# Kernel optimization log

Measured on AMD Instinct MI355X. Metric: run time of the kernel, lower is better.

## Reference

```python
import jax, jax.numpy as jnp
import numpy as np

HIDDEN = 1024
HEADS = 16
HEAD_DIM = HIDDEN // HEADS


def setup_inputs() -> dict:
    key = jax.random.key(0)
    ks = jax.random.split(key, 7)
    B, S = 4, 2048
    xav = float(np.sqrt(6.0 / (HIDDEN + HIDDEN)))  # xavier uniform bound
    def lin(k):
        return jax.random.uniform(k, (HIDDEN, HIDDEN), jnp.float32, -xav, xav)
    return {
        "hidden_states": jax.random.normal(ks[0], (B, S, HIDDEN), jnp.float32),
        "Wq": lin(ks[1]), "bq": jnp.zeros((HIDDEN,), jnp.float32),
        "Wk": lin(ks[2]), "bk": jnp.zeros((HIDDEN,), jnp.float32),
        "Wv": lin(ks[3]), "bv": jnp.zeros((HIDDEN,), jnp.float32),
    }


def reference(hidden_states, Wq, bq, Wk, bk, Wv, bv):
    B, S, H = hidden_states.shape
    def split_heads(t):  # [B,S,H] -> [B,heads,S,head_dim]
        return t.reshape(B, S, HEADS, HEAD_DIM).transpose(0, 2, 1, 3)
    q = split_heads(hidden_states @ Wq + bq)
    k = split_heads(hidden_states @ Wk + bk)
    v = split_heads(hidden_states @ Wv + bv)
    scores = jnp.einsum("bhqd,bhkd->bhqk", q, k) / jnp.sqrt(
        jnp.asarray(HEAD_DIM, hidden_states.dtype))
    probs = jax.nn.softmax(scores, axis=-1)  # dropout p=0.0 (inference)
    ctx = jnp.einsum("bhqk,bhkd->bhqd", probs, v)
    ctx = ctx.transpose(0, 2, 1, 3).reshape(B, S, H)
    return ctx
```

## Files before the change

kernel.cpp:

```cpp
#include <hip/hip_runtime.h>
#include <hip/hip_bf16.h>
#include <cstdint>

#define HIDDEN 1024
#define HEADS 16
#define HDIM 64
#define BATCH 4
#define SEQ 2048
#define MTOT (BATCH * SEQ)

typedef __attribute__((ext_vector_type(8))) short bfrag;
typedef __attribute__((ext_vector_type(4))) float cfrag;
typedef __attribute__((ext_vector_type(4))) float float4v;
typedef __attribute__((ext_vector_type(4))) unsigned short ushort4v;
typedef __attribute__((ext_vector_type(2))) unsigned int uint2v;

#define AS1 __attribute__((address_space(1)))
#define AS3 __attribute__((address_space(3)))

__device__ __forceinline__ void gl_lds16(const void* g, void* l) {
  __builtin_amdgcn_global_load_lds((AS1 void*)g, (AS3 void*)l, 16, 0, 0);
}

__device__ __forceinline__ uint16_t f2b(float f) {
  union { float f; uint32_t u; } v; v.f = f;
  uint32_t u = v.u;
  return (uint16_t)((u + 0x7FFFu + ((u >> 16) & 1u)) >> 16);
}

__global__ __launch_bounds__(256) void cvt_kernel(
    const float* __restrict__ x, const float* __restrict__ W0,
    const float* __restrict__ W1, const float* __restrict__ W2,
    uint16_t* __restrict__ Xb, uint16_t* __restrict__ Wt) {
  int bid = blockIdx.x;
  if (bid < 4096) {
    int i = bid * 256 + threadIdx.x;
    float4v a = ((const float4v*)x)[2 * i];
    float4v b = ((const float4v*)x)[2 * i + 1];
    bfrag o;
    o[0] = (short)f2b(a[0]); o[1] = (short)f2b(a[1]);
    o[2] = (short)f2b(a[2]); o[3] = (short)f2b(a[3]);
    o[4] = (short)f2b(b[0]); o[5] = (short)f2b(b[1]);
    o[6] = (short)f2b(b[2]); o[7] = (short)f2b(b[3]);
    ((bfrag*)Xb)[i] = o;
    return;
  }
  int id = bid - 4096;
  int z = id >> 8, rem = id & 255;
  const float* W = z == 0 ? W0 : (z == 1 ? W1 : W2);
  uint16_t* out = Wt + (size_t)z * HIDDEN * HIDDEN;
  __shared__ float tile[64][65];
  int n0 = (rem & 15) * 64, k0 = (rem >> 4) * 64;
  int t = threadIdx.x;
  int r = t >> 2, cq = (t & 3) * 16;
#pragma unroll
  for (int i = 0; i < 16; i += 4) {
    float4v v = *(const float4v*)&W[(size_t)(k0 + r) * HIDDEN + n0 + cq + i];
    tile[r][cq + i + 0] = v[0]; tile[r][cq + i + 1] = v[1];
    tile[r][cq + i + 2] = v[2]; tile[r][cq + i + 3] = v[3];
  }
  __syncthreads();
  bfrag o0, o1;
#pragma unroll
  for (int i = 0; i < 8; ++i) o0[i] = (short)f2b(tile[cq + i][r]);
#pragma unroll
  for (int i = 0; i < 8; ++i) o1[i] = (short)f2b(tile[cq + 8 + i][r]);
  *(bfrag*)&out[(size_t)(n0 + r) * HIDDEN + k0 + cq] = o0;
  *(bfrag*)&out[(size_t)(n0 + r) * HIDDEN + k0 + cq + 8] = o1;
}

__global__ __launch_bounds__(256) void gemm_qkv_kernel(
    const uint16_t* __restrict__ X, const uint16_t* __restrict__ Wt,
    const float* __restrict__ b0, const float* __restrict__ b1,
    const float* __restrict__ b2,
    uint16_t* __restrict__ Qo, uint16_t* __restrict__ Ko, uint16_t* __restrict__ Vo) {
  __shared__ uint16_t As[2][128 * 32];
  __shared__ uint16_t Bs[2][128 * 32];

  int id = blockIdx.x;
  int xcd = id & 7, j = id >> 3;
  int which = j >> 6;
  int r_ = j & 63;
  int m0 = (xcd * 8 + (r_ >> 3)) * 128;
  int n0 = (r_ & 7) * 128;

  const uint16_t* Wp = Wt + (size_t)which * HIDDEN * HIDDEN;
  const float* bias = which == 0 ? b0 : (which == 1 ? b1 : b2);

  int tid = threadIdx.x;
  int wave = tid >> 6, lane = tid & 63;
  int wm = wave >> 1, wn = wave & 1;
  int g = lane >> 4, c = lane & 15;
  int sr = lane >> 2;
  int sc = (lane & 3) * 8;

  cfrag acc[4][4];
#pragma unroll
  for (int i = 0; i < 4; ++i)
#pragma unroll
    for (int jj = 0; jj < 4; ++jj) acc[i][jj] = cfrag{0.f, 0.f, 0.f, 0.f};

  auto STAGE = [&](int buf, int kt) {
    int kc = kt * 32 + sc;
#pragma unroll
    for (int i = 0; i < 2; ++i) {
      int rowA = (i * 4 + wave) * 16;
      gl_lds16(&X[(size_t)(m0 + rowA + sr) * HIDDEN + kc], &As[buf][rowA * 32]);
      gl_lds16(&Wp[(size_t)(n0 + rowA + sr) * HIDDEN + kc], &Bs[buf][rowA * 32]);
    }
  };

  STAGE(0, 0);
  __syncthreads();
  int cur = 0;

  for (int kt = 0; kt < HIDDEN / 32; ++kt) {
    if (kt < HIDDEN / 32 - 1) STAGE(cur ^ 1, kt + 1);
    bfrag af[4], bf[4];
#pragma unroll
    for (int mt = 0; mt < 4; ++mt)
      af[mt] = *(const bfrag*)&As[cur][(wm * 64 + mt * 16 + c) * 32 + g * 8];
#pragma unroll
    for (int nt = 0; nt < 4; ++nt)
      bf[nt] = *(const bfrag*)&Bs[cur][(wn * 64 + nt * 16 + c) * 32 + g * 8];
    __builtin_amdgcn_s_setprio(1);
#pragma unroll
    for (int mt = 0; mt < 4; ++mt)
#pragma unroll
      for (int nt = 0; nt < 4; ++nt)
        acc[mt][nt] = __builtin_amdgcn_mfma_f32_16x16x32_bf16(af[mt], bf[nt],
                                                              acc[mt][nt], 0, 0, 0);
    __builtin_amdgcn_s_setprio(0);
    __syncthreads();
    cur ^= 1;
  }

  if (which == 2) {
    int bb_ = m0 >> 11;
    int s0 = (m0 & 2047) + wm * 64;
#pragma unroll
    for (int nt = 0; nt < 4; ++nt) {
      int n = n0 + wn * 64 + nt * 16 + c;
      int h = n >> 6, d = n & 63;
      float bb = bias[n];
      size_t base = ((size_t)(bb_ * 16 + h) * 64 + d) * SEQ;
#pragma unroll
      for (int mt = 0; mt < 4; ++mt) {
        int s = s0 + mt * 16 + g * 4;
        ushort4v pk;
        pk[0] = f2b(acc[mt][nt][0] + bb);
        pk[1] = f2b(acc[mt][nt][1] + bb);
        pk[2] = f2b(acc[mt][nt][2] + bb);
        pk[3] = f2b(acc[mt][nt][3] + bb);
        *(ushort4v*)&Vo[base + s] = pk;
      }
    }
  } else {
    uint16_t* out = which == 0 ? Qo : Ko;
    float sc_ = which == 0 ? 0.125f * 1.44269504088896f : 1.0f;
#pragma unroll
    for (int nt = 0; nt < 4; ++nt) {
      int n = n0 + wn * 64 + nt * 16 + c;
      float bb = bias[n];
#pragma unroll
      for (int mt = 0; mt < 4; ++mt) {
        int mb = m0 + wm * 64 + mt * 16 + g * 4;
#pragma unroll
        for (int r = 0; r < 4; ++r)
          out[(size_t)(mb + r) * HIDDEN + n] = f2b((acc[mt][nt][r] + bb) * sc_);
      }
    }
  }
}

__global__ __launch_bounds__(256, 4) void attn_kernel(
    const uint16_t* __restrict__ Q, const uint16_t* __restrict__ K,
    const uint16_t* __restrict__ VT, float* __restrict__ out) {
  __shared__ uint16_t Ks[2][64 * 64];
  __shared__ uint16_t Vs[2][64 * 64];
  __shared__ __align__(16) uint16_t Pl[4][16][64];

  int bid = blockIdx.x;
  int wg = (bid & 7) * 256 + (bid >> 3);
  int bh = wg >> 5, qt = wg & 31;
  int b = bh >> 4, h = bh & 15;
  int tid = threadIdx.x, wave = tid >> 6, lane = tid & 63;
  int g = lane >> 4, c = lane & 15;
  size_t rowb = (size_t)b * SEQ;
  int colb = h * HDIM;
  const uint16_t* Kh = K + rowb * HIDDEN + colb;
  const uint16_t* Vh = VT + (size_t)bh * HDIM * SEQ;

  int r8 = lane >> 3, c8 = lane & 7;
  int scol = ((c8 ^ r8) << 3);
  int sbrow = (wave & 1) * 32;

  int qrow = qt * 64 + wave * 16 + c;
  bfrag aq[2];
  aq[0] = *(const bfrag*)&Q[(rowb + qrow) * HIDDEN + colb + g * 8];
  aq[1] = *(const bfrag*)&Q[(rowb + qrow) * HIDDEN + colb + 32 + g * 8];

  float mr = -INFINITY, lr = 0.f;
  cfrag oacc[4];
#pragma unroll
  for (int dt = 0; dt < 4; ++dt) oacc[dt] = cfrag{0.f, 0.f, 0.f, 0.f};

  if (wave < 2) {
#pragma unroll
    for (int j = 0; j < 4; ++j) {
      int rl = sbrow + j * 8;
      gl_lds16(&Kh[(size_t)(rl + r8) * HIDDEN + scol], &Ks[0][rl * 64]);
    }
  } else {
#pragma unroll
    for (int j = 0; j < 4; ++j) {
      int rl = sbrow + j * 8;
      gl_lds16(&Vh[(size_t)(rl + r8) * SEQ + scol], &Vs[0][rl * 64]);
    }
  }
  __syncthreads();

  int cur = 0;
  int sw = (c & 7) << 4;
  uint8_t* Pb = (uint8_t*)Pl + wave * 2048 + c * 128;

  for (int t = 0; t < 32; ++t) {
    int j0 = t * 64;
    if (t < 31) {
      int jn = j0 + 64;
      if (wave < 2) {
#pragma unroll
        for (int j = 0; j < 4; ++j) {
          int rl = sbrow + j * 8;
          gl_lds16(&Kh[(size_t)(jn + rl + r8) * HIDDEN + scol],
                   &Ks[cur ^ 1][rl * 64]);
        }
      } else {
#pragma unroll
        for (int j = 0; j < 4; ++j) {
          int rl = sbrow + j * 8;
          gl_lds16(&Vh[(size_t)(rl + r8) * SEQ + jn + scol],
                   &Vs[cur ^ 1][rl * 64]);
        }
      }
    }

    const uint8_t* Kbuf = (const uint8_t*)Ks[cur];
    const uint8_t* Vbuf = (const uint8_t*)Vs[cur];

    cfrag s[4];
#pragma unroll
    for (int nt = 0; nt < 4; ++nt) s[nt] = cfrag{0.f, 0.f, 0.f, 0.f};
    __builtin_amdgcn_s_setprio(1);
#pragma unroll
    for (int kb = 0; kb < 2; ++kb) {
#pragma unroll
      for (int nt = 0; nt < 4; ++nt) {
        int off = ((nt * 16 + c) * 128 + kb * 64 + g * 16) ^ sw;
        bfrag bk = *(const bfrag*)(Kbuf + off);
        s[nt] = __builtin_amdgcn_mfma_f32_16x16x32_bf16(bk, aq[kb], s[nt], 0, 0, 0);
      }
    }
    __builtin_amdgcn_s_setprio(0);

    float mx = fmaxf(fmaxf(s[0][0], s[0][1]), s[0][2]);
    mx = fmaxf(fmaxf(mx, s[0][3]), s[1][0]);
    mx = fmaxf(fmaxf(mx, s[1][1]), s[1][2]);
    mx = fmaxf(fmaxf(mx, s[1][3]), s[2][0]);
    mx = fmaxf(fmaxf(mx, s[2][1]), s[2][2]);
    mx = fmaxf(fmaxf(mx, s[2][3]), s[3][0]);
    mx = fmaxf(fmaxf(mx, s[3][1]), s[3][2]);
    mx = fmaxf(mx, s[3][3]);
    mx = fmaxf(mx, __shfl_xor(mx, 16, 64));
    mx = fmaxf(mx, __shfl_xor(mx, 32, 64));
    if (mx > mr + 8.0f) {
      float alpha = __builtin_amdgcn_exp2f(mr - mx);
      lr *= alpha;
#pragma unroll
      for (int dt = 0; dt < 4; ++dt)
#pragma unroll
        for (int r = 0; r < 4; ++r) oacc[dt][r] *= alpha;
      mr = mx;
    }
    float ps = 0.f;
#pragma unroll
    for (int nt = 0; nt < 4; ++nt) {
#pragma unroll
      for (int r = 0; r < 4; ++r)
        s[nt][r] = __builtin_amdgcn_exp2f(s[nt][r] - mr);
      ps += (s[nt][0] + s[nt][1]) + (s[nt][2] + s[nt][3]);
    }
    lr += ps;

#pragma unroll
    for (int nt = 0; nt < 4; ++nt) {
      uint32_t w0, w1;
      asm("v_cvt_pk_bf16_f32 %0, %1, %2" : "=v"(w0) : "v"(s[nt][0]), "v"(s[nt][1]));
      asm("v_cvt_pk_bf16_f32 %0, %1, %2" : "=v"(w1) : "v"(s[nt][2]), "v"(s[nt][3]));
      uint2v pw; pw[0] = w0; pw[1] = w1;
      *(uint2v*)(Pb + ((nt * 32 + g * 8) ^ sw)) = pw;
    }

    __builtin_amdgcn_s_setprio(1);
#pragma unroll
    for (int kb = 0; kb < 2; ++kb) {
      bfrag ap = *(const bfrag*)(Pb + ((kb * 64 + g * 16) ^ sw));
#pragma unroll
      for (int dt = 0; dt < 4; ++dt) {
        int off = ((dt * 16 + c) * 128 + kb * 64 + g * 16) ^ sw;
        bfrag bv = *(const bfrag*)(Vbuf + off);
        oacc[dt] = __builtin_amdgcn_mfma_f32_16x16x32_bf16(bv, ap, oacc[dt], 0, 0, 0);
      }
    }
    __builtin_amdgcn_s_setprio(0);

    __syncthreads();
    cur ^= 1;
  }

  lr += __shfl_xor(lr, 16, 64);
  lr += __shfl_xor(lr, 32, 64);
  float inv = 1.0f / lr;
  size_t orow = rowb + (size_t)qt * 64 + wave * 16 + c;
#pragma unroll
  for (int dt = 0; dt < 4; ++dt) {
    float4v o;
    o[0] = oacc[dt][0] * inv; o[1] = oacc[dt][1] * inv;
    o[2] = oacc[dt][2] * inv; o[3] = oacc[dt][3] * inv;
    *(float4v*)&out[orow * HIDDEN + colb + dt * 16 + g * 4] = o;
  }
}

extern "C" void kernel_launch(void* const* d_in, const int* in_sizes, int n_in,
                              void* d_out, int out_size, void* d_ws, size_t ws_size,
                              hipStream_t stream) {
  const float* x  = (const float*)d_in[0];
  const float* Wq = (const float*)d_in[1];
  const float* bq = (const float*)d_in[2];
  const float* Wk = (const float*)d_in[3];
  const float* bk = (const float*)d_in[4];
  const float* Wv = (const float*)d_in[5];
  const float* bv = (const float*)d_in[6];
  float* out = (float*)d_out;

  uint8_t* ws = (uint8_t*)d_ws;
  const size_t XB = 0;
  const size_t WT = XB + (size_t)MTOT * HIDDEN * 2;
  const size_t QB = WT + (size_t)3 * HIDDEN * HIDDEN * 2;
  const size_t KB = QB + (size_t)MTOT * HIDDEN * 2;
  const size_t VB = KB + (size_t)MTOT * HIDDEN * 2;
  uint16_t* Xb = (uint16_t*)(ws + XB);
  uint16_t* Wt = (uint16_t*)(ws + WT);
  uint16_t* Qb = (uint16_t*)(ws + QB);
  uint16_t* Kb = (uint16_t*)(ws + KB);
  uint16_t* Vb = (uint16_t*)(ws + VB);

  cvt_kernel<<<dim3(4096 + 768), 256, 0, stream>>>(x, Wq, Wk, Wv, Xb, Wt);
  gemm_qkv_kernel<<<dim3(1536), 256, 0, stream>>>(Xb, Wt, bq, bk, bv, Qb, Kb, Vb);
  attn_kernel<<<dim3(2048), 256, 0, stream>>>(Qb, Kb, Vb, out);
}
```

Measured before the change: 284.7 us.

## Double query rows per attention wave and simplify QKV GEMM to single-buffered grid

The attention kernel now has each wave handle 32 query rows as two 16-row halves. Each K/V tile loaded into LDS is reused across twice as many queries, which halves the grid and the K/V traffic per query. The cost is more registers, so occupancy drops from 4 to 3 blocks. The QKV GEMM goes the other way: it drops double-buffered LDS prefetch, the XCD-aware block remap and the priority hints in favour of a plain 3D grid, which exposes global-to-LDS load latency on every k-step.

```diff
diff --git a/kernel.cpp b/kernel.cpp
--- a/kernel.cpp
+++ b/kernel.cpp
@@ -74,19 +74,13 @@
     const float* __restrict__ b0, const float* __restrict__ b1,
     const float* __restrict__ b2,
     uint16_t* __restrict__ Qo, uint16_t* __restrict__ Ko, uint16_t* __restrict__ Vo) {
-  __shared__ uint16_t As[2][128 * 32];
-  __shared__ uint16_t Bs[2][128 * 32];
-
-  int id = blockIdx.x;
-  int xcd = id & 7, j = id >> 3;
-  int which = j >> 6;
-  int r_ = j & 63;
-  int m0 = (xcd * 8 + (r_ >> 3)) * 128;
-  int n0 = (r_ & 7) * 128;
-
+  __shared__ uint16_t As[128 * 32];
+  __shared__ uint16_t Bs[128 * 32];
+  int which = blockIdx.z;
   const uint16_t* Wp = Wt + (size_t)which * HIDDEN * HIDDEN;
   const float* bias = which == 0 ? b0 : (which == 1 ? b1 : b2);
 
+  int m0 = blockIdx.x * 128, n0 = blockIdx.y * 128;
   int tid = threadIdx.x;
   int wave = tid >> 6, lane = tid & 63;
   int wm = wave >> 1, wn = wave & 1;
@@ -100,39 +94,29 @@
 #pragma unroll
     for (int jj = 0; jj < 4; ++jj) acc[i][jj] = cfrag{0.f, 0.f, 0.f, 0.f};
 
-  auto STAGE = [&](int buf, int kt) {
+  for (int kt = 0; kt < HIDDEN / 32; ++kt) {
     int kc = kt * 32 + sc;
 #pragma unroll
     for (int i = 0; i < 2; ++i) {
       int rowA = (i * 4 + wave) * 16;
-      gl_lds16(&X[(size_t)(m0 + rowA + sr) * HIDDEN + kc], &As[buf][rowA * 32]);
-      gl_lds16(&Wp[(size_t)(n0 + rowA + sr) * HIDDEN + kc], &Bs[buf][rowA * 32]);
-    }
-  };
-
-  STAGE(0, 0);
-  __syncthreads();
-  int cur = 0;
-
-  for (int kt = 0; kt < HIDDEN / 32; ++kt) {
-    if (kt < HIDDEN / 32 - 1) STAGE(cur ^ 1, kt + 1);
+      gl_lds16(&X[(size_t)(m0 + rowA + sr) * HIDDEN + kc], &As[rowA * 32]);
+      gl_lds16(&Wp[(size_t)(n0 + rowA + sr) * HIDDEN + kc], &Bs[rowA * 32]);
+    }
+    __syncthreads();
     bfrag af[4], bf[4];
 #pragma unroll
     for (int mt = 0; mt < 4; ++mt)
-      af[mt] = *(const bfrag*)&As[cur][(wm * 64 + mt * 16 + c) * 32 + g * 8];
+      af[mt] = *(const bfrag*)&As[(wm * 64 + mt * 16 + c) * 32 + g * 8];
 #pragma unroll
     for (int nt = 0; nt < 4; ++nt)
-      bf[nt] = *(const bfrag*)&Bs[cur][(wn * 64 + nt * 16 + c) * 32 + g * 8];
-    __builtin_amdgcn_s_setprio(1);
+      bf[nt] = *(const bfrag*)&Bs[(wn * 64 + nt * 16 + c) * 32 + g * 8];
 #pragma unroll
     for (int mt = 0; mt < 4; ++mt)
 #pragma unroll
       for (int nt = 0; nt < 4; ++nt)
         acc[mt][nt] = __builtin_amdgcn_mfma_f32_16x16x32_bf16(af[mt], bf[nt],
                                                               acc[mt][nt], 0, 0, 0);
-    __builtin_amdgcn_s_setprio(0);
     __syncthreads();
-    cur ^= 1;
   }
 
   if (which == 2) {
@@ -173,16 +157,16 @@
   }
 }
 
-__global__ __launch_bounds__(256, 4) void attn_kernel(
+__global__ __launch_bounds__(256, 3) void attn_kernel(
     const uint16_t* __restrict__ Q, const uint16_t* __restrict__ K,
     const uint16_t* __restrict__ VT, float* __restrict__ out) {
   __shared__ uint16_t Ks[2][64 * 64];
   __shared__ uint16_t Vs[2][64 * 64];
-  __shared__ __align__(16) uint16_t Pl[4][16][64];
+  __shared__ __align__(16) uint16_t Pl[4][32][64];
 
   int bid = blockIdx.x;
-  int wg = (bid & 7) * 256 + (bid >> 3);
-  int bh = wg >> 5, qt = wg & 31;
+  int wg = (bid & 7) * 128 + (bid >> 3);
+  int bh = wg >> 4, qt = wg & 15;
   int b = bh >> 4, h = bh & 15;
   int tid = threadIdx.x, wave = tid >> 6, lane = tid & 63;
   int g = lane >> 4, c = lane & 15;
@@ -195,15 +179,22 @@
   int scol = ((c8 ^ r8) << 3);
   int sbrow = (wave & 1) * 32;
 
-  int qrow = qt * 64 + wave * 16 + c;
-  bfrag aq[2];
-  aq[0] = *(const bfrag*)&Q[(rowb + qrow) * HIDDEN + colb + g * 8];
-  aq[1] = *(const bfrag*)&Q[(rowb + qrow) * HIDDEN + colb + 32 + g * 8];
-
-  float mr = -INFINITY, lr = 0.f;
-  cfrag oacc[4];
-#pragma unroll
-  for (int dt = 0; dt < 4; ++dt) oacc[dt] = cfrag{0.f, 0.f, 0.f, 0.f};
+  int qrow = qt * 128 + wave * 32 + c;
+  bfrag aq0[2], aq1[2];
+#pragma unroll
+  for (int kb = 0; kb < 2; ++kb) {
+    aq0[kb] = *(const bfrag*)&Q[(rowb + qrow) * HIDDEN + colb + kb * 32 + g * 8];
+    aq1[kb] = *(const bfrag*)&Q[(rowb + qrow + 16) * HIDDEN + colb + kb * 32 + g * 8];
+  }
+
+  float mr0 = -INFINITY, lr0 = 0.f;
+  float mr1 = -INFINITY, lr1 = 0.f;
+  cfrag oacc0[4], oacc1[4];
+#pragma unroll
+  for (int dt = 0; dt < 4; ++dt) {
+    oacc0[dt] = cfrag{0.f, 0.f, 0.f, 0.f};
+    oacc1[dt] = cfrag{0.f, 0.f, 0.f, 0.f};
+  }
 
   if (wave < 2) {
 #pragma unroll
@@ -222,7 +213,8 @@
 
   int cur = 0;
   int sw = (c & 7) << 4;
-  uint8_t* Pb = (uint8_t*)Pl + wave * 2048 + c * 128;
+  uint8_t* Pb0 = (uint8_t*)Pl + wave * 4096 + c * 128;
+  uint8_t* Pb1 = Pb0 + 16 * 128;
 
   for (int t = 0; t < 32; ++t) {
     int j0 = t * 64;
@@ -248,9 +240,12 @@
     const uint8_t* Kbuf = (const uint8_t*)Ks[cur];
     const uint8_t* Vbuf = (const uint8_t*)Vs[cur];
 
-    cfrag s[4];
-#pragma unroll
-    for (int nt = 0; nt < 4; ++nt) s[nt] = cfrag{0.f, 0.f, 0.f, 0.f};
+    cfrag s0[4], s1[4];
+#pragma unroll
+    for (int nt = 0; nt < 4; ++nt) {
+      s0[nt] = cfrag{0.f, 0.f, 0.f, 0.f};
+      s1[nt] = cfrag{0.f, 0.f, 0.f, 0.f};
+    }
     __builtin_amdgcn_s_setprio(1);
 #pragma unroll
     for (int kb = 0; kb < 2; ++kb) {
@@ -258,58 +253,100 @@
       for (int nt = 0; nt < 4; ++nt) {
         int off = ((nt * 16 + c) * 128 + kb * 64 + g * 16) ^ sw;
         bfrag bk = *(const bfrag*)(Kbuf + off);
-        s[nt] = __builtin_amdgcn_mfma_f32_16x16x32_bf16(bk, aq[kb], s[nt], 0, 0, 0);
+        s0[nt] = __builtin_amdgcn_mfma_f32_16x16x32_bf16(bk, aq0[kb], s0[nt], 0, 0, 0);
+        s1[nt] = __builtin_amdgcn_mfma_f32_16x16x32_bf16(bk, aq1[kb], s1[nt], 0, 0, 0);
       }
     }
     __builtin_amdgcn_s_setprio(0);
 
-    float mx = fmaxf(fmaxf(s[0][0], s[0][1]), s[0][2]);
-    mx = fmaxf(fmaxf(mx, s[0][3]), s[1][0]);
-    mx = fmaxf(fmaxf(mx, s[1][1]), s[1][2]);
-    mx = fmaxf(fmaxf(mx, s[1][3]), s[2][0]);
-    mx = fmaxf(fmaxf(mx, s[2][1]), s[2][2]);
-    mx = fmaxf(fmaxf(mx, s[2][3]), s[3][0]);
-    mx = fmaxf(fmaxf(mx, s[3][1]), s[3][2]);
-    mx = fmaxf(mx, s[3][3]);
-    mx = fmaxf(mx, __shfl_xor(mx, 16, 64));
-    mx = fmaxf(mx, __shfl_xor(mx, 32, 64));
-    if (mx > mr + 8.0f) {
-      float alpha = __builtin_amdgcn_exp2f(mr - mx);
-      lr *= alpha;
-#pragma unroll
-      for (int dt = 0; dt < 4; ++dt)
-#pragma unroll
-        for (int r = 0; r < 4; ++r) oacc[dt][r] *= alpha;
-      mr = mx;
-    }
-    float ps = 0.f;
-#pragma unroll
-    for (int nt = 0; nt < 4; ++nt) {
-#pragma unroll
-      for (int r = 0; r < 4; ++r)
-        s[nt][r] = __builtin_amdgcn_exp2f(s[nt][r] - mr);
-      ps += (s[nt][0] + s[nt][1]) + (s[nt][2] + s[nt][3]);
-    }
-    lr += ps;
-
-#pragma unroll
-    for (int nt = 0; nt < 4; ++nt) {
-      uint32_t w0, w1;
-      asm("v_cvt_pk_bf16_f32 %0, %1, %2" : "=v"(w0) : "v"(s[nt][0]), "v"(s[nt][1]));
-      asm("v_cvt_pk_bf16_f32 %0, %1, %2" : "=v"(w1) : "v"(s[nt][2]), "v"(s[nt][3]));
-      uint2v pw; pw[0] = w0; pw[1] = w1;
-      *(uint2v*)(Pb + ((nt * 32 + g * 8) ^ sw)) = pw;
+    {
+      float mx = fmaxf(fmaxf(s0[0][0], s0[0][1]), s0[0][2]);
+      mx = fmaxf(fmaxf(mx, s0[0][3]), s0[1][0]);
+      mx = fmaxf(fmaxf(mx, s0[1][1]), s0[1][2]);
+      mx = fmaxf(fmaxf(mx, s0[1][3]), s0[2][0]);
+      mx = fmaxf(fmaxf(mx, s0[2][1]), s0[2][2]);
+      mx = fmaxf(fmaxf(mx, s0[2][3]), s0[3][0]);
+      mx = fmaxf(fmaxf(mx, s0[3][1]), s0[3][2]);
+      mx = fmaxf(mx, s0[3][3]);
+      mx = fmaxf(mx, __shfl_xor(mx, 16, 64));
+      mx = fmaxf(mx, __shfl_xor(mx, 32, 64));
+      if (mx > mr0 + 8.0f) {
+        float alpha = __builtin_amdgcn_exp2f(mr0 - mx);
+        lr0 *= alpha;
+#pragma unroll
+        for (int dt = 0; dt < 4; ++dt)
+#pragma unroll
+          for (int r = 0; r < 4; ++r) oacc0[dt][r] *= alpha;
+        mr0 = mx;
+      }
+      float ps = 0.f;
+#pragma unroll
+      for (int nt = 0; nt < 4; ++nt) {
+#pragma unroll
+        for (int r = 0; r < 4; ++r)
+          s0[nt][r] = __builtin_amdgcn_exp2f(s0[nt][r] - mr0);
+        ps += (s0[nt][0] + s0[nt][1]) + (s0[nt][2] + s0[nt][3]);
+      }
+      lr0 += ps;
+#pragma unroll
+      for (int nt = 0; nt < 4; ++nt) {
+        uint32_t w0, w1;
+        asm("v_cvt_pk_bf16_f32 %0, %1, %2" : "=v"(w0) : "v"(s0[nt][0]), "v"(s0[nt][1]));
+        asm("v_cvt_pk_bf16_f32 %0, %1, %2" : "=v"(w1) : "v"(s0[nt][2]), "v"(s0[nt][3]));
+        uint2v pw; pw[0] = w0; pw[1] = w1;
+        *(uint2v*)(Pb0 + ((nt * 32 + g * 8) ^ sw)) = pw;
+      }
+    }
+    {
+      float mx = fmaxf(fmaxf(s1[0][0], s1[0][1]), s1[0][2]);
+      mx = fmaxf(fmaxf(mx, s1[0][3]), s1[1][0]);
+      mx = fmaxf(fmaxf(mx, s1[1][1]), s1[1][2]);
+      mx = fmaxf(fmaxf(mx, s1[1][3]), s1[2][0]);
+      mx = fmaxf(fmaxf(mx, s1[2][1]), s1[2][2]);
+      mx = fmaxf(fmaxf(mx, s1[2][3]), s1[3][0]);
+      mx = fmaxf(fmaxf(mx, s1[3][1]), s1[3][2]);
+      mx = fmaxf(mx, s1[3][3]);
+      mx = fmaxf(mx, __shfl_xor(mx, 16, 64));
+      mx = fmaxf(mx, __shfl_xor(mx, 32, 64));
+      if (mx > mr1 + 8.0f) {
+        float alpha = __builtin_amdgcn_exp2f(mr1 - mx);
+        lr1 *= alpha;
+#pragma unroll
+        for (int dt = 0; dt < 4; ++dt)
+#pragma unroll
+          for (int r = 0; r < 4; ++r) oacc1[dt][r] *= alpha;
+        mr1 = mx;
+      }
+      float ps = 0.f;
+#pragma unroll
+      for (int nt = 0; nt < 4; ++nt) {
+#pragma unroll
+        for (int r = 0; r < 4; ++r)
+          s1[nt][r] = __builtin_amdgcn_exp2f(s1[nt][r] - mr1);
+        ps += (s1[nt][0] + s1[nt][1]) + (s1[nt][2] + s1[nt][3]);
+      }
+      lr1 += ps;
+#pragma unroll
+      for (int nt = 0; nt < 4; ++nt) {
+        uint32_t w0, w1;
+        asm("v_cvt_pk_bf16_f32 %0, %1, %2" : "=v"(w0) : "v"(s1[nt][0]), "v"(s1[nt][1]));
+        asm("v_cvt_pk_bf16_f32 %0, %1, %2" : "=v"(w1) : "v"(s1[nt][2]), "v"(s1[nt][3]));
+        uint2v pw; pw[0] = w0; pw[1] = w1;
+        *(uint2v*)(Pb1 + ((nt * 32 + g * 8) ^ sw)) = pw;
+      }
     }
 
     __builtin_amdgcn_s_setprio(1);
 #pragma unroll
     for (int kb = 0; kb < 2; ++kb) {
-      bfrag ap = *(const bfrag*)(Pb + ((kb * 64 + g * 16) ^ sw));
+      bfrag ap0 = *(const bfrag*)(Pb0 + ((kb * 64 + g * 16) ^ sw));
+      bfrag ap1 = *(const bfrag*)(Pb1 + ((kb * 64 + g * 16) ^ sw));
 #pragma unroll
       for (int dt = 0; dt < 4; ++dt) {
         int off = ((dt * 16 + c) * 128 + kb * 64 + g * 16) ^ sw;
         bfrag bv = *(const bfrag*)(Vbuf + off);
-        oacc[dt] = __builtin_amdgcn_mfma_f32_16x16x32_bf16(bv, ap, oacc[dt], 0, 0, 0);
+        oacc0[dt] = __builtin_amdgcn_mfma_f32_16x16x32_bf16(bv, ap0, oacc0[dt], 0, 0, 0);
+        oacc1[dt] = __builtin_amdgcn_mfma_f32_16x16x32_bf16(bv, ap1, oacc1[dt], 0, 0, 0);
       }
     }
     __builtin_amdgcn_s_setprio(0);
@@ -318,16 +355,22 @@
     cur ^= 1;
   }
 
-  lr += __shfl_xor(lr, 16, 64);
-  lr += __shfl_xor(lr, 32, 64);
-  float inv = 1.0f / lr;
-  size_t orow = rowb + (size_t)qt * 64 + wave * 16 + c;
+  lr0 += __shfl_xor(lr0, 16, 64);
+  lr0 += __shfl_xor(lr0, 32, 64);
+  lr1 += __shfl_xor(lr1, 16, 64);
+  lr1 += __shfl_xor(lr1, 32, 64);
+  float inv0 = 1.0f / lr0, inv1 = 1.0f / lr1;
+  size_t orow = rowb + (size_t)qt * 128 + wave * 32 + c;
 #pragma unroll
   for (int dt = 0; dt < 4; ++dt) {
     float4v o;
-    o[0] = oacc[dt][0] * inv; o[1] = oacc[dt][1] * inv;
-    o[2] = oacc[dt][2] * inv; o[3] = oacc[dt][3] * inv;
+    o[0] = oacc0[dt][0] * inv0; o[1] = oacc0[dt][1] * inv0;
+    o[2] = oacc0[dt][2] * inv0; o[3] = oacc0[dt][3] * inv0;
     *(float4v*)&out[orow * HIDDEN + colb + dt * 16 + g * 4] = o;
+    float4v p;
+    p[0] = oacc1[dt][0] * inv1; p[1] = oacc1[dt][1] * inv1;
+    p[2] = oacc1[dt][2] * inv1; p[3] = oacc1[dt][3] * inv1;
+    *(float4v*)&out[(orow + 16) * HIDDEN + colb + dt * 16 + g * 4] = p;
   }
 }
 
@@ -356,6 +399,6 @@
   uint16_t* Vb = (uint16_t*)(ws + VB);
 
   cvt_kernel<<<dim3(4096 + 768), 256, 0, stream>>>(x, Wq, Wk, Wv, Xb, Wt);
-  gemm_qkv_kernel<<<dim3(1536), 256, 0, stream>>>(Xb, Wt, bq, bk, bv, Qb, Kb, Vb);
-  attn_kernel<<<dim3(2048), 256, 0, stream>>>(Qb, Kb, Vb, out);
-}
+  gemm_qkv_kernel<<<dim3(64, 8, 3), 256, 0, stream>>>(Xb, Wt, bq, bk, bv, Qb, Kb, Vb);
+  attn_kernel<<<dim3(1024), 256, 0, stream>>>(Qb, Kb, Vb, out);
+}
```

Measured after the change: 272.9 us. 1.04x faster.
